# Optimization experiments

Measured on AMD Instinct MI355X. Metric: run time of the kernel, lower is better.

## Reference

```python
import jax, jax.numpy as jnp
import numpy as np

B, S, D, H = 2, 2048, 1024, 16
DK = D // H

def setup_inputs() -> dict:
    key = jax.random.key(0)
    ks = jax.random.split(key, 11)
    scale = 1.0 / np.sqrt(D)
    inp = {
        'query': jax.random.normal(ks[0], (B, S, D), jnp.float32),
        'key':   jax.random.normal(ks[1], (B, S, D), jnp.float32),
        'value': jax.random.normal(ks[2], (B, S, D), jnp.float32),
        'wq': jax.random.normal(ks[3], (D, D), jnp.float32) * scale,
        'bq': jax.random.normal(ks[4], (D,), jnp.float32) * 0.01,
        'wk': jax.random.normal(ks[5], (D, D), jnp.float32) * scale,
        'bk': jax.random.normal(ks[6], (D,), jnp.float32) * 0.01,
        'wv': jax.random.normal(ks[7], (D, D), jnp.float32) * scale,
        'bv': jax.random.normal(ks[8], (D,), jnp.float32) * 0.01,
        'wo': jax.random.normal(ks[9], (D, D), jnp.float32) * scale,
        'bo': jax.random.normal(ks[10], (D,), jnp.float32) * 0.01,
    }
    return inp

def reference(query, key, value, wq, bq, wk, bk, wv, bv, wo, bo):
    nb = query.shape[0]
    # projections: torch nn.Linear computes x @ W^T + b; here weights stored as (in,out)
    def proj(x, w, b):
        return (x @ w + b).reshape(nb, -1, H, DK).transpose(0, 2, 1, 3)  # [B,H,S,dk]
    q = proj(query, wq, bq)
    k = proj(key, wk, bk)
    v = proj(value, wv, bv)
    scores = jnp.einsum('bhqd,bhkd->bhqk', q, k) / jnp.sqrt(jnp.float32(DK))
    p = jax.nn.softmax(scores, axis=-1)  # dropout p=0 (eval)
    x = jnp.einsum('bhqk,bhkd->bhqd', p, v)
    x = x.transpose(0, 2, 1, 3).reshape(nb, -1, H * DK)
    return x @ wo + bo
```

## Files before the change

kernel.cpp:

```cpp
#include <hip/hip_runtime.h>


typedef __attribute__((ext_vector_type(8))) __bf16 bf16x8;
typedef __attribute__((ext_vector_type(4))) __bf16 bf16x4;
typedef __attribute__((ext_vector_type(8))) float f32x8;
typedef __attribute__((ext_vector_type(4))) float f32x4;
typedef unsigned uv2 __attribute__((ext_vector_type(2)));

#define MFMA16 __builtin_amdgcn_mfma_f32_16x16x32_bf16

union Bf8 { bf16x8 v; __bf16 e[8]; };

__device__ inline f32x4 zero4() { f32x4 z; z[0]=z[1]=z[2]=z[3]=0.f; return z; }

__device__ inline float fast_exp2(float x) {
#if __has_builtin(__builtin_amdgcn_exp2f)
    return __builtin_amdgcn_exp2f(x);
#else
    return __expf(x * 0.6931471805599453f);
#endif
}

#if __has_builtin(__builtin_amdgcn_permlane16_swap) && __has_builtin(__builtin_amdgcn_permlane32_swap)
#define HAVE_PLSWAP 1
#endif

__device__ inline float red16_max(float x) {
#ifdef HAVE_PLSWAP
    uv2 r = __builtin_amdgcn_permlane16_swap(__float_as_uint(x), __float_as_uint(x), false, false);
    return fmaxf(__uint_as_float(r[0]), __uint_as_float(r[1]));
#else
    return fmaxf(x, __shfl_xor(x, 16));
#endif
}
__device__ inline float red32_max(float x) {
#ifdef HAVE_PLSWAP
    uv2 r = __builtin_amdgcn_permlane32_swap(__float_as_uint(x), __float_as_uint(x), false, false);
    return fmaxf(__uint_as_float(r[0]), __uint_as_float(r[1]));
#else
    return fmaxf(x, __shfl_xor(x, 32));
#endif
}
__device__ inline float red16_sum(float x) {
#ifdef HAVE_PLSWAP
    uv2 r = __builtin_amdgcn_permlane16_swap(__float_as_uint(x), __float_as_uint(x), false, false);
    return __uint_as_float(r[0]) + __uint_as_float(r[1]);
#else
    return x + __shfl_xor(x, 16);
#endif
}
__device__ inline float red32_sum(float x) {
#ifdef HAVE_PLSWAP
    uv2 r = __builtin_amdgcn_permlane32_swap(__float_as_uint(x), __float_as_uint(x), false, false);
    return __uint_as_float(r[0]) + __uint_as_float(r[1]);
#else
    return x + __shfl_xor(x, 32);
#endif
}

__device__ inline void load_lds16(const void* g, void* l) {
    __builtin_amdgcn_global_load_lds(
        (const __attribute__((address_space(1))) unsigned int*)g,
        (__attribute__((address_space(3))) unsigned int*)l, 16, 0, 0);
}

__global__ __launch_bounds__(256) void prep_all(
        const float* __restrict__ w0, const float* __restrict__ w1,
        const float* __restrict__ w2, const float* __restrict__ w3,
        const float* __restrict__ x0, const float* __restrict__ x1,
        const float* __restrict__ x2,
        __bf16* __restrict__ wt, __bf16* __restrict__ d0,
        __bf16* __restrict__ d1, __bf16* __restrict__ d2) {
    const int z = blockIdx.z, t = threadIdx.x;
    if (z < 4) {
        const float* src = z == 0 ? w0 : z == 1 ? w1 : z == 2 ? w2 : w3;
        __bf16* dst = wt + (size_t)z * 1048576;
        __shared__ float tile[32][33];
        const int tc = t & 31, tr = t >> 5;
        const int r0 = blockIdx.y * 32, c0 = blockIdx.x * 32;
#pragma unroll
        for (int i = 0; i < 4; i++) {
            int r = tr + i * 8;
            tile[r][tc] = src[(size_t)(r0 + r) * 1024 + c0 + tc];
        }
        __syncthreads();
#pragma unroll
        for (int i = 0; i < 4; i++) {
            int r = tr + i * 8;
            dst[(size_t)(c0 + r) * 1024 + r0 + tc] = (__bf16)tile[tc][r];
        }
    } else {
        const float* src = z == 4 ? x0 : z == 5 ? x1 : x2;
        __bf16* dst = z == 4 ? d0 : z == 5 ? d1 : d2;
        int bid = blockIdx.y * 32 + blockIdx.x;
        size_t g = ((size_t)bid * 256 + t) * 16;
#pragma unroll
        for (int h = 0; h < 2; h++) {
            f32x8 a = *(const f32x8*)&src[g + h * 8];
            Bf8 tmp;
#pragma unroll
            for (int j = 0; j < 8; j++) tmp.e[j] = (__bf16)a[j];
            *(bf16x8*)&dst[g + h * 8] = tmp.v;
        }
    }
}

template <int MODE, typename OutT>
__device__ inline void gemm_fast_core(__bf16* __restrict__ smem,
                                      const __bf16* __restrict__ A,
                                      const __bf16* __restrict__ Bt,
                                      const float* __restrict__ bias,
                                      OutT* __restrict__ out, float scale) {
    __bf16* As = smem;
    __bf16* Bs = smem + 8192;
    const int t = threadIdx.x;
    const int wave = t >> 6, lane = t & 63, lm = lane & 15, quad = lane >> 4;
    const int m0 = blockIdx.y * 128, n0 = blockIdx.x * 128;
    const int wm = (wave >> 1) * 64, wn = (wave & 1) * 64;

    f32x4 acc[4][4];
#pragma unroll
    for (int i = 0; i < 4; i++)
#pragma unroll
        for (int j = 0; j < 4; j++) acc[i][j] = zero4();

    for (int k0 = 0; k0 < 1024; k0 += 64) {
#pragma unroll
        for (int i = 0; i < 4; i++) {
            int s = i * 256 + t;
            int row = s >> 3, cb = (s & 7) ^ (row & 7);
            size_t goff = (size_t)row * 1024 + k0 + cb * 8;
            load_lds16(&A[(size_t)m0 * 1024 + goff],
                       &As[(size_t)(i * 256 + wave * 64) * 8]);
            load_lds16(&Bt[(size_t)n0 * 1024 + goff],
                       &Bs[(size_t)(i * 256 + wave * 64) * 8]);
        }
        __syncthreads();
#pragma unroll
        for (int ks = 0; ks < 2; ks++) {
            bf16x8 af[4], bfr[4];
#pragma unroll
            for (int mt = 0; mt < 4; mt++)
                af[mt] = *(const bf16x8*)&As[(wm + mt * 16 + lm) * 64 +
                                             (((ks * 4 + quad) ^ (lm & 7)) * 8)];
#pragma unroll
            for (int nt = 0; nt < 4; nt++)
                bfr[nt] = *(const bf16x8*)&Bs[(wn + nt * 16 + lm) * 64 +
                                              (((ks * 4 + quad) ^ (lm & 7)) * 8)];
#pragma unroll
            for (int mt = 0; mt < 4; mt++)
#pragma unroll
                for (int nt = 0; nt < 4; nt++)
                    acc[mt][nt] = MFMA16(af[mt], bfr[nt], acc[mt][nt], 0, 0, 0);
        }
        __syncthreads();
    }

    float bv4[4];
#pragma unroll
    for (int nt = 0; nt < 4; nt++) bv4[nt] = bias[n0 + wn + nt * 16 + lm];

    if (MODE == 2) {
#pragma unroll
        for (int mt = 0; mt < 4; mt++)
#pragma unroll
            for (int r = 0; r < 4; r++) {
                int rr = wm + mt * 16 + quad * 4 + r;
#pragma unroll
                for (int nt = 0; nt < 4; nt++) {
                    int c = wn + nt * 16 + lm;
                    smem[c * 128 + (rr ^ (8 * (c & 15)))] =
                        (__bf16)((acc[mt][nt][r] + bv4[nt]) * scale);
                }
            }
        __syncthreads();
        const int b = m0 >> 11;
#pragma unroll
        for (int it = 0; it < 8; it++) {
            int g = it * 256 + t;
            int c = g >> 4, gr = g & 15;
            bf16x8 v = *(const bf16x8*)&smem[c * 128 + ((gr * 8) ^ (8 * (c & 15)))];
            int col = n0 + c, hh = col >> 6, dk = col & 63;
            int sglob = (m0 & 2047) + gr * 8;
            size_t idx = (size_t)(b * 16 + hh) * 131072 + (size_t)dk * 2048 + sglob;
            *(bf16x8*)&out[idx] = v;
        }
    } else {
#pragma unroll
        for (int mt = 0; mt < 4; mt++) {
#pragma unroll
            for (int r = 0; r < 4; r++) {
                int row = m0 + wm + mt * 16 + quad * 4 + r;
#pragma unroll
                for (int nt = 0; nt < 4; nt++) {
                    int col = n0 + wn + nt * 16 + lm;
                    float val = (acc[mt][nt][r] + bv4[nt]) * scale;
                    size_t idx;
                    if (MODE == 0) {
                        idx = (size_t)row * 1024 + col;
                    } else {
                        int b = row >> 11, s = row & 2047, hh = col >> 6, dk = col & 63;
                        idx = (size_t)(b * 16 + hh) * 131072 + (size_t)s * 64 + dk;
                    }
                    out[idx] = (OutT)val;
                }
            }
        }
    }
}

__global__ __launch_bounds__(256) void proj_fast3(
        const __bf16* __restrict__ xq, const __bf16* __restrict__ xk,
        const __bf16* __restrict__ xv, const __bf16* __restrict__ WT,
        const float* __restrict__ bq, const float* __restrict__ bk,
        const float* __restrict__ bv,
        __bf16* __restrict__ Q, __bf16* __restrict__ K, __bf16* __restrict__ Vt) {
    __shared__ __bf16 smem[16384];
    int z = blockIdx.z;
    if (z == 0)
        gemm_fast_core<1, __bf16>(smem, xq, WT, bq, Q, 0.18033688f);
    else if (z == 1)
        gemm_fast_core<1, __bf16>(smem, xk, WT + 1048576, bk, K, 1.f);
    else
        gemm_fast_core<2, __bf16>(smem, xv, WT + 2097152, bv, Vt, 1.f);
}

__global__ __launch_bounds__(256) void out_proj_fast64(
        const __bf16* __restrict__ A, const __bf16* __restrict__ Bt,
        const float* __restrict__ bias, float* __restrict__ out) {
    __shared__ __bf16 As[8192];
    __shared__ __bf16 Bs[4096];
    const int t = threadIdx.x;
    const int wave = t >> 6, lane = t & 63, lm = lane & 15, quad = lane >> 4;
    const int m0 = blockIdx.y * 128, n0 = blockIdx.x * 64;
    const int wm = (wave >> 1) * 64, wn = (wave & 1) * 32;

    f32x4 acc[4][2];
#pragma unroll
    for (int i = 0; i < 4; i++) { acc[i][0] = zero4(); acc[i][1] = zero4(); }

    for (int k0 = 0; k0 < 1024; k0 += 64) {
#pragma unroll
        for (int i = 0; i < 4; i++) {
            int s = i * 256 + t;
            int row = s >> 3, cb = (s & 7) ^ (row & 7);
            load_lds16(&A[(size_t)(m0 + row) * 1024 + k0 + cb * 8],
                       &As[(size_t)(i * 256 + wave * 64) * 8]);
            if (i < 2)
                load_lds16(&Bt[(size_t)(n0 + row) * 1024 + k0 + cb * 8],
                           &Bs[(size_t)(i * 256 + wave * 64) * 8]);
        }
        __syncthreads();
#pragma unroll
        for (int ks = 0; ks < 2; ks++) {
            bf16x8 af[4], bfr[2];
#pragma unroll
            for (int mt = 0; mt < 4; mt++)
                af[mt] = *(const bf16x8*)&As[(wm + mt * 16 + lm) * 64 +
                                             (((ks * 4 + quad) ^ (lm & 7)) * 8)];
#pragma unroll
            for (int nt = 0; nt < 2; nt++)
                bfr[nt] = *(const bf16x8*)&Bs[(wn + nt * 16 + lm) * 64 +
                                              (((ks * 4 + quad) ^ (lm & 7)) * 8)];
#pragma unroll
            for (int mt = 0; mt < 4; mt++)
#pragma unroll
                for (int nt = 0; nt < 2; nt++)
                    acc[mt][nt] = MFMA16(af[mt], bfr[nt], acc[mt][nt], 0, 0, 0);
        }
        __syncthreads();
    }

    float bv2[2];
#pragma unroll
    for (int nt = 0; nt < 2; nt++) bv2[nt] = bias[n0 + wn + nt * 16 + lm];

#pragma unroll
    for (int mt = 0; mt < 4; mt++)
#pragma unroll
        for (int r = 0; r < 4; r++) {
            int row = m0 + wm + mt * 16 + quad * 4 + r;
#pragma unroll
            for (int nt = 0; nt < 2; nt++) {
                int col = n0 + wn + nt * 16 + lm;
                out[(size_t)row * 1024 + col] = acc[mt][nt][r] + bv2[nt];
            }
        }
}

__global__ __launch_bounds__(256, 2) void attn_kernel(
        const __bf16* __restrict__ Q, const __bf16* __restrict__ K,
        const __bf16* __restrict__ Vt, __bf16* __restrict__ O) {
    __shared__ __bf16 Ks[2][4096];
    __shared__ __bf16 Vs[2][4096];
    __shared__ __bf16 Ps[4 * 32 * 72];
    const int t = threadIdx.x;
    const int wave = t >> 6, lane = t & 63, lm = lane & 15, quad = lane >> 4;
    const int q0 = blockIdx.x * 128;
    const int bh = blockIdx.y;
    const size_t base = (size_t)bh * 131072;

    bf16x8 bq[2][2];
    {
        int qrow = q0 + wave * 32;
#pragma unroll
        for (int nt = 0; nt < 2; nt++)
#pragma unroll
            for (int ks = 0; ks < 2; ks++)
                bq[nt][ks] = *(const bf16x8*)
                    &Q[base + (size_t)(qrow + nt * 16 + lm) * 64 + ks * 32 + quad * 8];
    }

    float m_run[2], l_run[2];
#pragma unroll
    for (int n = 0; n < 2; n++) { m_run[n] = -1e30f; l_run[n] = 0.f; }
    f32x4 o_acc[4][2];
#pragma unroll
    for (int mt = 0; mt < 4; mt++)
#pragma unroll
        for (int n = 0; n < 2; n++) o_acc[mt][n] = zero4();

    __bf16* Pw = &Ps[wave * 32 * 72];

    auto stageK = [&](int buf, int kv0) {
#pragma unroll
        for (int i = 0; i < 2; i++) {
            int s = i * 256 + t;
            int row = s >> 3, cb = (s & 7) ^ (row & 7);
            load_lds16(&K[base + (size_t)(kv0 + row) * 64 + cb * 8],
                       &Ks[buf][(i * 256 + wave * 64) * 8]);
        }
    };
    auto stageV = [&](int buf, int kv0) {
#pragma unroll
        for (int i = 0; i < 2; i++) {
            int s = i * 256 + t;
            int row = s >> 3, cb = (s & 7) ^ (row & 7);
            load_lds16(&Vt[base + (size_t)row * 2048 + kv0 + cb * 8],
                       &Vs[buf][(i * 256 + wave * 64) * 8]);
        }
    };

    auto pv_step = [&](int pbuf) {
#pragma unroll
        for (int ks = 0; ks < 2; ks++) {
            bf16x8 bp[2];
#pragma unroll
            for (int nt = 0; nt < 2; nt++)
                bp[nt] = *(const bf16x8*)&Pw[(nt * 16 + lm) * 72 + ks * 32 + quad * 8];
#pragma unroll
            for (int mt = 0; mt < 4; mt++) {
                bf16x8 av = *(const bf16x8*)&Vs[pbuf][(mt * 16 + lm) * 64 +
                                                (((ks * 4 + quad) ^ (lm & 7)) * 8)];
                o_acc[mt][0] = MFMA16(av, bp[0], o_acc[mt][0], 0, 0, 0);
                o_acc[mt][1] = MFMA16(av, bp[1], o_acc[mt][1], 0, 0, 0);
            }
        }
    };

    stageK(0, 0);
    __syncthreads();

    for (int it = 0; it < 32; ++it) {
        const int cur = it & 1;
        if (it < 31) stageK(cur ^ 1, (it + 1) * 64);
        stageV(cur, it * 64);

        f32x4 sc[4][2];
        __builtin_amdgcn_s_setprio(1);
#pragma unroll
        for (int mt = 0; mt < 4; mt++) {
            sc[mt][0] = zero4();
            sc[mt][1] = zero4();
#pragma unroll
            for (int ks = 0; ks < 2; ks++) {
                bf16x8 ak = *(const bf16x8*)&Ks[cur][(mt * 16 + lm) * 64 +
                                                (((ks * 4 + quad) ^ (lm & 7)) * 8)];
                sc[mt][0] = MFMA16(ak, bq[0][ks], sc[mt][0], 0, 0, 0);
                sc[mt][1] = MFMA16(ak, bq[1][ks], sc[mt][1], 0, 0, 0);
            }
        }
        if (it > 0) pv_step(cur ^ 1);
        __builtin_amdgcn_s_setprio(0);
        __asm__ volatile("" ::: "memory");

#pragma unroll
        for (int nt = 0; nt < 2; nt++) {
            float mx = -1e30f;
#pragma unroll
            for (int mt = 0; mt < 4; mt++)
#pragma unroll
                for (int r = 0; r < 4; r++) mx = fmaxf(mx, sc[mt][nt][r]);
            mx = red32_max(red16_max(mx));
            float mo = m_run[nt];
            if (__all(mx <= mo + 8.f)) {
                float su = 0.f;
#pragma unroll
                for (int mt = 0; mt < 4; mt++)
#pragma unroll
                    for (int r = 0; r < 4; r++) {
                        float p = fast_exp2(sc[mt][nt][r] - mo);
                        sc[mt][nt][r] = p;
                        su += p;
                    }
                l_run[nt] += red32_sum(red16_sum(su));
            } else {
                float mn = fmaxf(mo, mx);
                float alpha = fast_exp2(mo - mn);
                m_run[nt] = mn;
                float su = 0.f;
#pragma unroll
                for (int mt = 0; mt < 4; mt++)
#pragma unroll
                    for (int r = 0; r < 4; r++) {
                        float p = fast_exp2(sc[mt][nt][r] - mn);
                        sc[mt][nt][r] = p;
                        su += p;
                    }
                l_run[nt] = l_run[nt] * alpha + red32_sum(red16_sum(su));
#pragma unroll
                for (int mt = 0; mt < 4; mt++)
#pragma unroll
                    for (int r = 0; r < 4; r++) o_acc[mt][nt][r] *= alpha;
            }
        }

#pragma unroll
        for (int nt = 0; nt < 2; nt++)
#pragma unroll
            for (int mt = 0; mt < 4; mt++) {
                bf16x4 pk;
#pragma unroll
                for (int r = 0; r < 4; r++) pk[r] = (__bf16)sc[mt][nt][r];
                *(bf16x4*)&Pw[(nt * 16 + lm) * 72 + mt * 16 + quad * 4] = pk;
            }
        __asm__ volatile("" ::: "memory");

        __syncthreads();
    }

    __builtin_amdgcn_s_setprio(1);
    pv_step(1);
    __builtin_amdgcn_s_setprio(0);

#pragma unroll
    for (int nt = 0; nt < 2; nt++) {
        float inv = 1.f / l_run[nt];
#pragma unroll
        for (int mt = 0; mt < 4; mt++) {
            bf16x4 pk;
#pragma unroll
            for (int r = 0; r < 4; r++) pk[r] = (__bf16)(o_acc[mt][nt][r] * inv);
            *(bf16x4*)&Pw[(nt * 16 + lm) * 72 + mt * 16 + quad * 4] = pk;
        }
    }
    __asm__ volatile("" ::: "memory");
    __syncthreads();
    {
        const int b = bh >> 4, h = bh & 15;
        int ql = lane >> 1, half = lane & 1;
        int srow = q0 + wave * 32 + ql;
#pragma unroll
        for (int j = 0; j < 4; j++) {
            bf16x8 v = *(const bf16x8*)&Pw[ql * 72 + half * 32 + j * 8];
            *(bf16x8*)&O[(size_t)(b * 2048 + srow) * 1024 + h * 64 + half * 32 + j * 8] = v;
        }
    }
}

extern "C" void kernel_launch(void* const* d_in, const int* in_sizes, int n_in,
                              void* d_out, int out_size, void* d_ws, size_t ws_size,
                              hipStream_t stream) {
    if (ws_size < ((size_t)40 << 20)) return;

    const float* query = (const float*)d_in[0];
    const float* key_  = (const float*)d_in[1];
    const float* value = (const float*)d_in[2];
    const float* wq = (const float*)d_in[3];
    const float* bq = (const float*)d_in[4];
    const float* wk = (const float*)d_in[5];
    const float* bk = (const float*)d_in[6];
    const float* wv = (const float*)d_in[7];
    const float* bv = (const float*)d_in[8];
    const float* wo = (const float*)d_in[9];
    const float* bo = (const float*)d_in[10];
    float* out = (float*)d_out;

    char* ws = (char*)d_ws;
    __bf16* WT  = (__bf16*)(ws);
    __bf16* Qw  = (__bf16*)(ws + ((size_t)8  << 20));
    __bf16* Kw  = (__bf16*)(ws + ((size_t)16 << 20));
    __bf16* Vtw = (__bf16*)(ws + ((size_t)24 << 20));
    __bf16* Ow  = (__bf16*)(ws + ((size_t)32 << 20));

    __bf16* Xq = Ow;
    __bf16* Xk = (__bf16*)d_out;
    __bf16* Xv = (__bf16*)d_out + 4194304;

    prep_all<<<dim3(32, 32, 7), dim3(256), 0, stream>>>(
        wq, wk, wv, wo, query, key_, value, WT, Xq, Xk, Xv);
    proj_fast3<<<dim3(8, 32, 3), dim3(256), 0, stream>>>(
        Xq, Xk, Xv, WT, bq, bk, bv, Qw, Kw, Vtw);
    attn_kernel<<<dim3(16, 32), dim3(256), 0, stream>>>(Qw, Kw, Vtw, Ow);
    out_proj_fast64<<<dim3(16, 32), dim3(256), 0, stream>>>(
        Ow, WT + 3 * 1048576, bo, out);
}
```

Before: 234.1 us.

## Switch attention to 32x32x16 MFMA and keep P in registers via permlane swaps

The attention kernel now uses 32x32x16 bf16 MFMAs instead of 16x16x32, so each lane holds a single query column, which simplifies the softmax reductions to one permlane32 swap. The probability tile is repacked in registers with permlane32_swap into the B-operand layout for the PV MFMA, removing the per-iteration LDS write and read of P. LDS is merged into one buffer that is reused for the output staging. The costs are larger accumulator register footprints and extra swap instructions.

```diff
diff --git a/kernel.cpp b/kernel.cpp
--- a/kernel.cpp
+++ b/kernel.cpp
@@ -5,13 +5,21 @@
 typedef __attribute__((ext_vector_type(4))) __bf16 bf16x4;
 typedef __attribute__((ext_vector_type(8))) float f32x8;
 typedef __attribute__((ext_vector_type(4))) float f32x4;
+typedef __attribute__((ext_vector_type(16))) float f32x16;
 typedef unsigned uv2 __attribute__((ext_vector_type(2)));
 
 #define MFMA16 __builtin_amdgcn_mfma_f32_16x16x32_bf16
+#define MFMA32 __builtin_amdgcn_mfma_f32_32x32x16_bf16
 
 union Bf8 { bf16x8 v; __bf16 e[8]; };
 
 __device__ inline f32x4 zero4() { f32x4 z; z[0]=z[1]=z[2]=z[3]=0.f; return z; }
+__device__ inline f32x16 zero16() {
+    f32x16 z;
+#pragma unroll
+    for (int i = 0; i < 16; i++) z[i] = 0.f;
+    return z;
+}
 
 __device__ inline float fast_exp2(float x) {
 #if __has_builtin(__builtin_amdgcn_exp2f)
@@ -21,41 +29,46 @@
 #endif
 }
 
-#if __has_builtin(__builtin_amdgcn_permlane16_swap) && __has_builtin(__builtin_amdgcn_permlane32_swap)
+#if __has_builtin(__builtin_amdgcn_permlane32_swap)
 #define HAVE_PLSWAP 1
 #endif
 
-__device__ inline float red16_max(float x) {
+__device__ inline void plswap32(unsigned &a, unsigned &b) {
 #ifdef HAVE_PLSWAP
-    uv2 r = __builtin_amdgcn_permlane16_swap(__float_as_uint(x), __float_as_uint(x), false, false);
-    return fmaxf(__uint_as_float(r[0]), __uint_as_float(r[1]));
+    uv2 r = __builtin_amdgcn_permlane32_swap(a, b, false, false);
+    a = r[0]; b = r[1];
 #else
-    return fmaxf(x, __shfl_xor(x, 16));
+    unsigned sa = __shfl_xor((int)a, 32), sb = __shfl_xor((int)b, 32);
+    bool hi = (threadIdx.x & 32) != 0;
+    unsigned na = hi ? sb : a;
+    unsigned nb = hi ? b : sa;
+    a = na; b = nb;
 #endif
 }
+
 __device__ inline float red32_max(float x) {
 #ifdef HAVE_PLSWAP
-    uv2 r = __builtin_amdgcn_permlane32_swap(__float_as_uint(x), __float_as_uint(x), false, false);
+    unsigned a = __float_as_uint(x), b = __float_as_uint(x);
+    uv2 r = __builtin_amdgcn_permlane32_swap(a, b, false, false);
     return fmaxf(__uint_as_float(r[0]), __uint_as_float(r[1]));
 #else
     return fmaxf(x, __shfl_xor(x, 32));
 #endif
 }
-__device__ inline float red16_sum(float x) {
-#ifdef HAVE_PLSWAP
-    uv2 r = __builtin_amdgcn_permlane16_swap(__float_as_uint(x), __float_as_uint(x), false, false);
-    return __uint_as_float(r[0]) + __uint_as_float(r[1]);
-#else
-    return x + __shfl_xor(x, 16);
-#endif
-}
 __device__ inline float red32_sum(float x) {
 #ifdef HAVE_PLSWAP
-    uv2 r = __builtin_amdgcn_permlane32_swap(__float_as_uint(x), __float_as_uint(x), false, false);
+    unsigned a = __float_as_uint(x), b = __float_as_uint(x);
+    uv2 r = __builtin_amdgcn_permlane32_swap(a, b, false, false);
     return __uint_as_float(r[0]) + __uint_as_float(r[1]);
 #else
     return x + __shfl_xor(x, 32);
 #endif
+}
+
+__device__ inline unsigned pk2(float a, float b) {
+    union { unsigned u; __bf16 e[2]; } r;
+    r.e[0] = (__bf16)a; r.e[1] = (__bf16)b;
+    return r.u;
 }
 
 __device__ inline void load_lds16(const void* g, void* l) {
@@ -291,36 +304,27 @@
 __global__ __launch_bounds__(256, 2) void attn_kernel(
         const __bf16* __restrict__ Q, const __bf16* __restrict__ K,
         const __bf16* __restrict__ Vt, __bf16* __restrict__ O) {
-    __shared__ __bf16 Ks[2][4096];
-    __shared__ __bf16 Vs[2][4096];
-    __shared__ __bf16 Ps[4 * 32 * 72];
+    __shared__ __bf16 smem[16384];
     const int t = threadIdx.x;
-    const int wave = t >> 6, lane = t & 63, lm = lane & 15, quad = lane >> 4;
+    const int wave = t >> 6, lane = t & 63;
+    const int l31 = lane & 31, h = lane >> 5;
     const int q0 = blockIdx.x * 128;
     const int bh = blockIdx.y;
     const size_t base = (size_t)bh * 131072;
 
-    bf16x8 bq[2][2];
+    bf16x8 bq[4];
     {
-        int qrow = q0 + wave * 32;
-#pragma unroll
-        for (int nt = 0; nt < 2; nt++)
-#pragma unroll
-            for (int ks = 0; ks < 2; ks++)
-                bq[nt][ks] = *(const bf16x8*)
-                    &Q[base + (size_t)(qrow + nt * 16 + lm) * 64 + ks * 32 + quad * 8];
-    }
-
-    float m_run[2], l_run[2];
-#pragma unroll
-    for (int n = 0; n < 2; n++) { m_run[n] = -1e30f; l_run[n] = 0.f; }
-    f32x4 o_acc[4][2];
-#pragma unroll
-    for (int mt = 0; mt < 4; mt++)
-#pragma unroll
-        for (int n = 0; n < 2; n++) o_acc[mt][n] = zero4();
-
-    __bf16* Pw = &Ps[wave * 32 * 72];
+        int qrow = q0 + wave * 32 + l31;
+#pragma unroll
+        for (int kst = 0; kst < 4; kst++)
+            bq[kst] = *(const bf16x8*)&Q[base + (size_t)qrow * 64 + kst * 16 + h * 8];
+    }
+
+    float m_run = -1e30f, l_run = 0.f;
+    f32x16 o_acc[2];
+    o_acc[0] = zero16();
+    o_acc[1] = zero16();
+    bf16x8 bp[4];
 
     auto stageK = [&](int buf, int kv0) {
 #pragma unroll
@@ -328,7 +332,7 @@
             int s = i * 256 + t;
             int row = s >> 3, cb = (s & 7) ^ (row & 7);
             load_lds16(&K[base + (size_t)(kv0 + row) * 64 + cb * 8],
-                       &Ks[buf][(i * 256 + wave * 64) * 8]);
+                       &smem[buf * 4096 + (i * 256 + wave * 64) * 8]);
         }
     };
     auto stageV = [&](int buf, int kv0) {
@@ -337,24 +341,7 @@
             int s = i * 256 + t;
             int row = s >> 3, cb = (s & 7) ^ (row & 7);
             load_lds16(&Vt[base + (size_t)row * 2048 + kv0 + cb * 8],
-                       &Vs[buf][(i * 256 + wave * 64) * 8]);
-        }
-    };
-
-    auto pv_step = [&](int pbuf) {
-#pragma unroll
-        for (int ks = 0; ks < 2; ks++) {
-            bf16x8 bp[2];
-#pragma unroll
-            for (int nt = 0; nt < 2; nt++)
-                bp[nt] = *(const bf16x8*)&Pw[(nt * 16 + lm) * 72 + ks * 32 + quad * 8];
-#pragma unroll
-            for (int mt = 0; mt < 4; mt++) {
-                bf16x8 av = *(const bf16x8*)&Vs[pbuf][(mt * 16 + lm) * 64 +
-                                                (((ks * 4 + quad) ^ (lm & 7)) * 8)];
-                o_acc[mt][0] = MFMA16(av, bp[0], o_acc[mt][0], 0, 0, 0);
-                o_acc[mt][1] = MFMA16(av, bp[1], o_acc[mt][1], 0, 0, 0);
-            }
+                       &smem[8192 + buf * 4096 + (i * 256 + wave * 64) * 8]);
         }
     };
 
@@ -366,104 +353,123 @@
         if (it < 31) stageK(cur ^ 1, (it + 1) * 64);
         stageV(cur, it * 64);
 
-        f32x4 sc[4][2];
+        const __bf16* Ksc = &smem[cur * 4096];
+        f32x16 sc[2];
+        sc[0] = zero16();
+        sc[1] = zero16();
         __builtin_amdgcn_s_setprio(1);
 #pragma unroll
-        for (int mt = 0; mt < 4; mt++) {
-            sc[mt][0] = zero4();
-            sc[mt][1] = zero4();
-#pragma unroll
-            for (int ks = 0; ks < 2; ks++) {
-                bf16x8 ak = *(const bf16x8*)&Ks[cur][(mt * 16 + lm) * 64 +
-                                                (((ks * 4 + quad) ^ (lm & 7)) * 8)];
-                sc[mt][0] = MFMA16(ak, bq[0][ks], sc[mt][0], 0, 0, 0);
-                sc[mt][1] = MFMA16(ak, bq[1][ks], sc[mt][1], 0, 0, 0);
+        for (int mtk = 0; mtk < 2; mtk++)
+#pragma unroll
+            for (int kst = 0; kst < 4; kst++) {
+                bf16x8 ak = *(const bf16x8*)&Ksc[(mtk * 32 + l31) * 64 +
+                                                 (((kst * 2 + h) ^ (l31 & 7)) * 8)];
+                sc[mtk] = MFMA32(ak, bq[kst], sc[mtk], 0, 0, 0);
             }
-        }
-        if (it > 0) pv_step(cur ^ 1);
+        if (it > 0) {
+            const __bf16* Vsc = &smem[8192 + (cur ^ 1) * 4096];
+#pragma unroll
+            for (int kb = 0; kb < 4; kb++)
+#pragma unroll
+                for (int mtd = 0; mtd < 2; mtd++) {
+                    bf16x8 av = *(const bf16x8*)&Vsc[(mtd * 32 + l31) * 64 +
+                                                     (((kb * 2 + h) ^ (l31 & 7)) * 8)];
+                    o_acc[mtd] = MFMA32(av, bp[kb], o_acc[mtd], 0, 0, 0);
+                }
+        }
         __builtin_amdgcn_s_setprio(0);
-        __asm__ volatile("" ::: "memory");
-
-#pragma unroll
-        for (int nt = 0; nt < 2; nt++) {
-            float mx = -1e30f;
-#pragma unroll
-            for (int mt = 0; mt < 4; mt++)
-#pragma unroll
-                for (int r = 0; r < 4; r++) mx = fmaxf(mx, sc[mt][nt][r]);
-            mx = red32_max(red16_max(mx));
-            float mo = m_run[nt];
-            if (__all(mx <= mo + 8.f)) {
-                float su = 0.f;
-#pragma unroll
-                for (int mt = 0; mt < 4; mt++)
-#pragma unroll
-                    for (int r = 0; r < 4; r++) {
-                        float p = fast_exp2(sc[mt][nt][r] - mo);
-                        sc[mt][nt][r] = p;
-                        su += p;
-                    }
-                l_run[nt] += red32_sum(red16_sum(su));
-            } else {
-                float mn = fmaxf(mo, mx);
-                float alpha = fast_exp2(mo - mn);
-                m_run[nt] = mn;
-                float su = 0.f;
-#pragma unroll
-                for (int mt = 0; mt < 4; mt++)
-#pragma unroll
-                    for (int r = 0; r < 4; r++) {
-                        float p = fast_exp2(sc[mt][nt][r] - mn);
-                        sc[mt][nt][r] = p;
-                        su += p;
-                    }
-                l_run[nt] = l_run[nt] * alpha + red32_sum(red16_sum(su));
-#pragma unroll
-                for (int mt = 0; mt < 4; mt++)
-#pragma unroll
-                    for (int r = 0; r < 4; r++) o_acc[mt][nt][r] *= alpha;
+
+        float mx = sc[0][0];
+#pragma unroll
+        for (int mtk = 0; mtk < 2; mtk++)
+#pragma unroll
+            for (int r = 0; r < 16; r++) mx = fmaxf(mx, sc[mtk][r]);
+        mx = red32_max(mx);
+        float mo = m_run;
+        if (__all(mx <= mo + 8.f)) {
+            float su = 0.f;
+#pragma unroll
+            for (int mtk = 0; mtk < 2; mtk++)
+#pragma unroll
+                for (int r = 0; r < 16; r++) {
+                    float p = fast_exp2(sc[mtk][r] - mo);
+                    sc[mtk][r] = p;
+                    su += p;
+                }
+            l_run += red32_sum(su);
+        } else {
+            float mn = fmaxf(mo, mx);
+            float alpha = fast_exp2(mo - mn);
+            m_run = mn;
+            float su = 0.f;
+#pragma unroll
+            for (int mtk = 0; mtk < 2; mtk++)
+#pragma unroll
+                for (int r = 0; r < 16; r++) {
+                    float p = fast_exp2(sc[mtk][r] - mn);
+                    sc[mtk][r] = p;
+                    su += p;
+                }
+            l_run = l_run * alpha + red32_sum(su);
+#pragma unroll
+            for (int mtd = 0; mtd < 2; mtd++)
+#pragma unroll
+                for (int r = 0; r < 16; r++) o_acc[mtd][r] *= alpha;
+        }
+
+#pragma unroll
+        for (int kb = 0; kb < 4; kb++) {
+            const int mt = kb >> 1, g = (kb & 1) * 2;
+            unsigned A0 = pk2(sc[mt][g * 4 + 0], sc[mt][g * 4 + 1]);
+            unsigned A1 = pk2(sc[mt][g * 4 + 2], sc[mt][g * 4 + 3]);
+            unsigned B0 = pk2(sc[mt][g * 4 + 4], sc[mt][g * 4 + 5]);
+            unsigned B1 = pk2(sc[mt][g * 4 + 6], sc[mt][g * 4 + 7]);
+            plswap32(A0, B0);
+            plswap32(A1, B1);
+            union { unsigned u[4]; bf16x8 v; } bb;
+            bb.u[0] = A0; bb.u[1] = A1; bb.u[2] = B0; bb.u[3] = B1;
+            bp[kb] = bb.v;
+        }
+
+        __syncthreads();
+    }
+
+    {
+        const __bf16* Vsc = &smem[8192 + 4096];
+        __builtin_amdgcn_s_setprio(1);
+#pragma unroll
+        for (int kb = 0; kb < 4; kb++)
+#pragma unroll
+            for (int mtd = 0; mtd < 2; mtd++) {
+                bf16x8 av = *(const bf16x8*)&Vsc[(mtd * 32 + l31) * 64 +
+                                                 (((kb * 2 + h) ^ (l31 & 7)) * 8)];
+                o_acc[mtd] = MFMA32(av, bp[kb], o_acc[mtd], 0, 0, 0);
             }
-        }
-
-#pragma unroll
-        for (int nt = 0; nt < 2; nt++)
-#pragma unroll
-            for (int mt = 0; mt < 4; mt++) {
-                bf16x4 pk;
-#pragma unroll
-                for (int r = 0; r < 4; r++) pk[r] = (__bf16)sc[mt][nt][r];
-                *(bf16x4*)&Pw[(nt * 16 + lm) * 72 + mt * 16 + quad * 4] = pk;
+        __builtin_amdgcn_s_setprio(0);
+    }
+    __syncthreads();
+
+    {
+        float inv = 1.f / l_run;
+        __bf16* Osc = &smem[wave * 2176];
+#pragma unroll
+        for (int mtd = 0; mtd < 2; mtd++)
+#pragma unroll
+            for (int c = 0; c < 4; c++) {
+                bf16x4 pk4;
+#pragma unroll
+                for (int r2 = 0; r2 < 4; r2++)
+                    pk4[r2] = (__bf16)(o_acc[mtd][c * 4 + r2] * inv);
+                *(bf16x4*)&Osc[l31 * 68 + mtd * 32 + c * 8 + h * 4] = pk4;
             }
         __asm__ volatile("" ::: "memory");
-
-        __syncthreads();
-    }
-
-    __builtin_amdgcn_s_setprio(1);
-    pv_step(1);
-    __builtin_amdgcn_s_setprio(0);
-
-#pragma unroll
-    for (int nt = 0; nt < 2; nt++) {
-        float inv = 1.f / l_run[nt];
-#pragma unroll
-        for (int mt = 0; mt < 4; mt++) {
-            bf16x4 pk;
-#pragma unroll
-            for (int r = 0; r < 4; r++) pk[r] = (__bf16)(o_acc[mt][nt][r] * inv);
-            *(bf16x4*)&Pw[(nt * 16 + lm) * 72 + mt * 16 + quad * 4] = pk;
-        }
-    }
-    __asm__ volatile("" ::: "memory");
-    __syncthreads();
-    {
-        const int b = bh >> 4, h = bh & 15;
+        const int b = bh >> 4, hh = bh & 15;
         int ql = lane >> 1, half = lane & 1;
         int srow = q0 + wave * 32 + ql;
 #pragma unroll
         for (int j = 0; j < 4; j++) {
-            bf16x8 v = *(const bf16x8*)&Pw[ql * 72 + half * 32 + j * 8];
-            *(bf16x8*)&O[(size_t)(b * 2048 + srow) * 1024 + h * 64 + half * 32 + j * 8] = v;
+            bf16x8 v = *(const bf16x8*)&Osc[ql * 68 + half * 32 + j * 8];
+            *(bf16x8*)&O[(size_t)(b * 2048 + srow) * 1024 + hh * 64 + half * 32 + j * 8] = v;
         }
     }
 }
```

Result: faster. 228.6 us (-2.3%).
